# Performance work log

Hardware: AMD Instinct MI355X
Metric: run time of the kernel (lower is better)

## Reference

```python
import jax, jax.numpy as jnp
import numpy as np


def setup_inputs() -> dict:
    key = jax.random.key(0)
    k1, k2 = jax.random.split(key)
    L = 4096000  # 160^3 mesh points
    B = 64       # receivers
    # mesh coordinates in a 10m x 8m x 3m room
    mesh_3D = jax.random.uniform(k1, (L, 3), dtype=jnp.float32) * jnp.array([10.0, 8.0, 3.0], jnp.float32)
    receiver_pos = jax.random.uniform(k2, (B, 3), dtype=jnp.float32) * jnp.array([10.0, 8.0, 3.0], jnp.float32)
    return {"mesh_3D": mesh_3D, "receiver_pos": receiver_pos}


def reference(mesh_3D, receiver_pos):
    # mesh_3D: (L, 3) flattened meshgrid; receiver_pos: (B, 3)
    mesh_flat = mesh_3D.reshape(-1, 3)                      # (L, 3)
    L = mesh_flat.shape[0]
    # Brute-force squared distances via ||m||^2 - 2 m.r + ||r||^2 -> (B, L)
    # (sqrt is monotone, argmin unchanged; distances themselves are not returned)
    m_sq = jnp.sum(mesh_flat * mesh_flat, axis=1)           # (L,)
    r_sq = jnp.sum(receiver_pos * receiver_pos, axis=1)     # (B,)
    cross = receiver_pos @ mesh_flat.T                      # (B, L)
    d2 = m_sq[None, :] - 2.0 * cross + r_sq[:, None]        # (B, L)
    min_idx = jnp.argmin(d2, axis=1)                        # (B,)
    one_hot = jnp.zeros((L,), mesh_flat.dtype).at[min_idx].set(1.0)
    closest_points = mesh_flat[min_idx]                     # (B, 3)
    input_tensor = jnp.concatenate([mesh_flat, one_hot[:, None]], axis=1)  # (L, 4)
    return input_tensor, closest_points
```

## Files before the change

### kernel.cpp

```cpp
#include <hip/hip_runtime.h>
#include <cfloat>
#include <math.h>
#include <stdint.h>

#pragma clang fp contract(off)

#define RPW 16
#define NQ  256
#define PPL 8
#define TILESZ (256 * PPL)

__device__ __forceinline__ uint32_t monotone_key(float f) {
    uint32_t u = __float_as_uint(f);
    return (u & 0x80000000u) ? ~u : (u | 0x80000000u);
}

__device__ __forceinline__ float rfl_f(float x) {
    return __uint_as_float((uint32_t)__builtin_amdgcn_readfirstlane((int)__float_as_uint(x)));
}

__device__ __forceinline__ unsigned long long shfl_xor_u64(unsigned long long v, int m) {
    uint32_t lo = (uint32_t)v, hi = (uint32_t)(v >> 32);
    lo = (uint32_t)__shfl_xor((int)lo, m, 64);
    hi = (uint32_t)__shfl_xor((int)hi, m, 64);
    return ((unsigned long long)hi << 32) | lo;
}

__global__ void __launch_bounds__(256, 4) fused_kernel(
        const float* __restrict__ mesh, const float* __restrict__ recv,
        float* __restrict__ out, unsigned long long* __restrict__ ws,
        int L, int B, int ntiles) {
    __shared__ unsigned long long wmin[4][RPW];

    const int tid  = threadIdx.x;
    const int lane = tid & 63;
    const int wave = tid >> 6;
    const int rq   = blockIdx.x / NQ;
    const int q0   = blockIdx.x % NQ;

    float rx[RPW], ry[RPW], rz[RPW], rsq[RPW];
#pragma unroll
    for (int c = 0; c < RPW; ++c) {
        const int r = rq * RPW + c;
        float x = 0.f, y = 0.f, z = 0.f;
        if (r < B) {
            x = recv[r * 3 + 0];
            y = recv[r * 3 + 1];
            z = recv[r * 3 + 2];
        }
        rx[c]  = rfl_f(x);
        ry[c]  = rfl_f(y);
        rz[c]  = rfl_f(z);
        rsq[c] = rfl_f((x * x + y * y) + z * z);
    }

    float    best[RPW];
    uint32_t grp[RPW];
#pragma unroll
    for (int c = 0; c < RPW; ++c) { best[c] = FLT_MAX; grp[c] = 0; }

    const bool writer = (rq == 0);

    for (int t = q0; t < ntiles; t += NQ) {
        const int p0 = t * TILESZ + (wave << 9) + (lane << 3);
        float xs[PPL], ys[PPL], zs[PPL], ms[PPL];
        if (p0 + PPL <= L) {
            const float4* __restrict__ m4 = (const float4*)(mesh + (size_t)p0 * 3);
            const float4 fa = m4[0], fb = m4[1], fc = m4[2];
            const float4 fd = m4[3], fe = m4[4], ff = m4[5];
            if (writer) {
                float4* __restrict__ o4 = (float4*)(out + (size_t)p0 * 4);
                o4[0] = make_float4(fa.x, fa.y, fa.z, 0.f);
                o4[1] = make_float4(fa.w, fb.x, fb.y, 0.f);
                o4[2] = make_float4(fb.z, fb.w, fc.x, 0.f);
                o4[3] = make_float4(fc.y, fc.z, fc.w, 0.f);
                o4[4] = make_float4(fd.x, fd.y, fd.z, 0.f);
                o4[5] = make_float4(fd.w, fe.x, fe.y, 0.f);
                o4[6] = make_float4(fe.z, fe.w, ff.x, 0.f);
                o4[7] = make_float4(ff.y, ff.z, ff.w, 0.f);
            }
            xs[0] = fa.x; ys[0] = fa.y; zs[0] = fa.z;
            xs[1] = fa.w; ys[1] = fb.x; zs[1] = fb.y;
            xs[2] = fb.z; ys[2] = fb.w; zs[2] = fc.x;
            xs[3] = fc.y; ys[3] = fc.z; zs[3] = fc.w;
            xs[4] = fd.x; ys[4] = fd.y; zs[4] = fd.z;
            xs[5] = fd.w; ys[5] = fe.x; zs[5] = fe.y;
            xs[6] = fe.z; ys[6] = fe.w; zs[6] = ff.x;
            xs[7] = ff.y; ys[7] = ff.z; zs[7] = ff.w;
#pragma unroll
            for (int j = 0; j < PPL; ++j)
                ms[j] = (xs[j] * xs[j] + ys[j] * ys[j]) + zs[j] * zs[j];
        } else {
#pragma unroll
            for (int j = 0; j < PPL; ++j) {
                const int p = p0 + j;
                if (p < L) {
                    xs[j] = mesh[(size_t)p * 3 + 0];
                    ys[j] = mesh[(size_t)p * 3 + 1];
                    zs[j] = mesh[(size_t)p * 3 + 2];
                    ms[j] = (xs[j] * xs[j] + ys[j] * ys[j]) + zs[j] * zs[j];
                    if (writer) {
                        out[(size_t)p * 4 + 0] = xs[j];
                        out[(size_t)p * 4 + 1] = ys[j];
                        out[(size_t)p * 4 + 2] = zs[j];
                        out[(size_t)p * 4 + 3] = 0.f;
                    }
                } else {
                    xs[j] = 0.f; ys[j] = 0.f; zs[j] = 0.f;
                    ms[j] = INFINITY;
                }
            }
        }

        const uint32_t g = (uint32_t)(p0 >> 3);
#pragma unroll
        for (int c = 0; c < RPW; ++c) {
            float v[PPL];
#pragma unroll
            for (int j = 0; j < PPL; ++j) {
                float cr = fmaf(rz[c], zs[j], fmaf(ry[c], ys[j], rx[c] * xs[j]));
                v[j] = fmaf(-2.0f, cr, ms[j]);
            }
            float a  = fminf(fminf(v[0], v[1]), v[2]);
            float b  = fminf(fminf(v[3], v[4]), v[5]);
            float cc = fminf(v[6], v[7]);
            float tl = fminf(fminf(a, b), cc);
            float d2g = tl + rsq[c];
            if (d2g < best[c]) { best[c] = d2g; grp[c] = g; }
        }
    }

#pragma unroll
    for (int c = 0; c < RPW; ++c) {
        unsigned long long kk =
            ((unsigned long long)monotone_key(best[c]) << 32) | grp[c];
#pragma unroll
        for (int off = 32; off >= 1; off >>= 1) {
            unsigned long long o = shfl_xor_u64(kk, off);
            if (o < kk) kk = o;
        }
        if (lane == 0) wmin[wave][c] = kk;
    }
    __syncthreads();
    if (tid < RPW) {
        unsigned long long kk = wmin[0][tid];
#pragma unroll
        for (int w = 1; w < 4; ++w) {
            unsigned long long o = wmin[w][tid];
            if (o < kk) kk = o;
        }
        const int r = rq * RPW + tid;
        if (r < B) atomicMin(&ws[r], kk);
    }
}

__global__ void finalize_kernel(
        const float* __restrict__ mesh, const float* __restrict__ recv,
        const unsigned long long* __restrict__ ws,
        float* __restrict__ out, int L, int B) {
    const int r = threadIdx.x;
    if (r >= B) return;
    const unsigned long long key = ws[r];
    const int p0 = (int)(key & 0xFFFFFFFFull) << 3;

    const float rx = recv[r * 3 + 0];
    const float ry = recv[r * 3 + 1];
    const float rz = recv[r * 3 + 2];
    const float rsq = (rx * rx + ry * ry) + rz * rz;

    float bestd = FLT_MAX;
    int   bidx  = p0;
    for (int j = 0; j < 8; ++j) {
        const int p = p0 + j;
        float d2;
        if (p < L) {
            const float x = mesh[(size_t)p * 3 + 0];
            const float y = mesh[(size_t)p * 3 + 1];
            const float z = mesh[(size_t)p * 3 + 2];
            const float ms = (x * x + y * y) + z * z;
            const float cr = fmaf(rz, z, fmaf(ry, y, rx * x));
            d2 = fmaf(-2.0f, cr, ms) + rsq;
        } else {
            d2 = INFINITY;
        }
        if (d2 < bestd) { bestd = d2; bidx = p; }
    }

    out[(size_t)bidx * 4 + 3] = 1.0f;
    float* cp = out + (size_t)L * 4 + (size_t)r * 3;
    cp[0] = mesh[(size_t)bidx * 3 + 0];
    cp[1] = mesh[(size_t)bidx * 3 + 1];
    cp[2] = mesh[(size_t)bidx * 3 + 2];
}

extern "C" void kernel_launch(void* const* d_in, const int* in_sizes, int n_in,
                              void* d_out, int out_size, void* d_ws, size_t ws_size,
                              hipStream_t stream) {
    const float* mesh = (const float*)d_in[0];
    const float* recv = (const float*)d_in[1];
    float* out = (float*)d_out;
    const int L = in_sizes[0] / 3;
    const int B = in_sizes[1] / 3;
    unsigned long long* ws = (unsigned long long*)d_ws;

    hipMemsetAsync(ws, 0xFF, (size_t)B * sizeof(unsigned long long), stream);

    const int ntiles = (L + TILESZ - 1) / TILESZ;
    fused_kernel<<<4 * NQ, 256, 0, stream>>>(mesh, recv, out, ws, L, B, ntiles);

    finalize_kernel<<<1, 64, 0, stream>>>(mesh, recv, ws, out, L, B);
}
```

Measured before the change: 61.26 us.

## Use packed FP32 FMA math and prefetch next mesh tile into registers

Rewrites the per-receiver distance computation to use two-wide float vectors, so the compiler can emit packed FMA instructions that handle two mesh points per instruction. It also software-pipelines the tile loop by issuing the next tile's six float4 loads before the compute on the current tile, hiding global load latency. The cost is more live registers for the prefetched tile and packing shuffles, which could pressure occupancy under the 4-wave launch bound.

```diff
diff --git a/kernel.cpp b/kernel.cpp
--- a/kernel.cpp
+++ b/kernel.cpp
@@ -4,6 +4,8 @@
 #include <stdint.h>
 
 #pragma clang fp contract(off)
+
+typedef float v2f __attribute__((ext_vector_type(2)));
 
 #define RPW 16
 #define NQ  256
@@ -24,6 +26,11 @@
     lo = (uint32_t)__shfl_xor((int)lo, m, 64);
     hi = (uint32_t)__shfl_xor((int)hi, m, 64);
     return ((unsigned long long)hi << 32) | lo;
+}
+
+__device__ __forceinline__ v2f sp(float s) { return (v2f){s, s}; }
+__device__ __forceinline__ v2f pkfma(v2f a, v2f b, v2f c) {
+    return __builtin_elementwise_fma(a, b, c);
 }
 
 __global__ void __launch_bounds__(256, 4) fused_kernel(
@@ -61,73 +68,100 @@
 
     const bool writer = (rq == 0);
 
-    for (int t = q0; t < ntiles; t += NQ) {
-        const int p0 = t * TILESZ + (wave << 9) + (lane << 3);
-        float xs[PPL], ys[PPL], zs[PPL], ms[PPL];
-        if (p0 + PPL <= L) {
-            const float4* __restrict__ m4 = (const float4*)(mesh + (size_t)p0 * 3);
-            const float4 fa = m4[0], fb = m4[1], fc = m4[2];
-            const float4 fd = m4[3], fe = m4[4], ff = m4[5];
+    float4 nb0, nb1, nb2, nb3, nb4, nb5;
+    int  t  = q0;
+    int  p0 = t * TILESZ + (wave << 9) + (lane << 3);
+    bool curFull = (t < ntiles) && (p0 + PPL <= L);
+    if (curFull) {
+        const float4* __restrict__ m4 = (const float4*)(mesh + (size_t)p0 * 3);
+        nb0 = m4[0]; nb1 = m4[1]; nb2 = m4[2];
+        nb3 = m4[3]; nb4 = m4[4]; nb5 = m4[5];
+    }
+
+    while (t < ntiles) {
+        v2f x2[4], y2[4], z2[4], ms2[4];
+        if (curFull) {
+            x2[0] = (v2f){nb0.x, nb0.w}; y2[0] = (v2f){nb0.y, nb1.x}; z2[0] = (v2f){nb0.z, nb1.y};
+            x2[1] = (v2f){nb1.z, nb2.y}; y2[1] = (v2f){nb1.w, nb2.z}; z2[1] = (v2f){nb2.x, nb2.w};
+            x2[2] = (v2f){nb3.x, nb3.w}; y2[2] = (v2f){nb3.y, nb4.x}; z2[2] = (v2f){nb3.z, nb4.y};
+            x2[3] = (v2f){nb4.z, nb5.y}; y2[3] = (v2f){nb4.w, nb5.z}; z2[3] = (v2f){nb5.x, nb5.w};
+#pragma unroll
+            for (int j = 0; j < 4; ++j)
+                ms2[j] = (x2[j] * x2[j] + y2[j] * y2[j]) + z2[j] * z2[j];
             if (writer) {
                 float4* __restrict__ o4 = (float4*)(out + (size_t)p0 * 4);
-                o4[0] = make_float4(fa.x, fa.y, fa.z, 0.f);
-                o4[1] = make_float4(fa.w, fb.x, fb.y, 0.f);
-                o4[2] = make_float4(fb.z, fb.w, fc.x, 0.f);
-                o4[3] = make_float4(fc.y, fc.z, fc.w, 0.f);
-                o4[4] = make_float4(fd.x, fd.y, fd.z, 0.f);
-                o4[5] = make_float4(fd.w, fe.x, fe.y, 0.f);
-                o4[6] = make_float4(fe.z, fe.w, ff.x, 0.f);
-                o4[7] = make_float4(ff.y, ff.z, ff.w, 0.f);
+                o4[0] = make_float4(x2[0].x, y2[0].x, z2[0].x, 0.f);
+                o4[1] = make_float4(x2[0].y, y2[0].y, z2[0].y, 0.f);
+                o4[2] = make_float4(x2[1].x, y2[1].x, z2[1].x, 0.f);
+                o4[3] = make_float4(x2[1].y, y2[1].y, z2[1].y, 0.f);
+                o4[4] = make_float4(x2[2].x, y2[2].x, z2[2].x, 0.f);
+                o4[5] = make_float4(x2[2].y, y2[2].y, z2[2].y, 0.f);
+                o4[6] = make_float4(x2[3].x, y2[3].x, z2[3].x, 0.f);
+                o4[7] = make_float4(x2[3].y, y2[3].y, z2[3].y, 0.f);
             }
-            xs[0] = fa.x; ys[0] = fa.y; zs[0] = fa.z;
-            xs[1] = fa.w; ys[1] = fb.x; zs[1] = fb.y;
-            xs[2] = fb.z; ys[2] = fb.w; zs[2] = fc.x;
-            xs[3] = fc.y; ys[3] = fc.z; zs[3] = fc.w;
-            xs[4] = fd.x; ys[4] = fd.y; zs[4] = fd.z;
-            xs[5] = fd.w; ys[5] = fe.x; zs[5] = fe.y;
-            xs[6] = fe.z; ys[6] = fe.w; zs[6] = ff.x;
-            xs[7] = ff.y; ys[7] = ff.z; zs[7] = ff.w;
-#pragma unroll
-            for (int j = 0; j < PPL; ++j)
-                ms[j] = (xs[j] * xs[j] + ys[j] * ys[j]) + zs[j] * zs[j];
         } else {
+            float xx[PPL], yy[PPL], zz[PPL], mm[PPL];
 #pragma unroll
             for (int j = 0; j < PPL; ++j) {
                 const int p = p0 + j;
                 if (p < L) {
-                    xs[j] = mesh[(size_t)p * 3 + 0];
-                    ys[j] = mesh[(size_t)p * 3 + 1];
-                    zs[j] = mesh[(size_t)p * 3 + 2];
-                    ms[j] = (xs[j] * xs[j] + ys[j] * ys[j]) + zs[j] * zs[j];
+                    xx[j] = mesh[(size_t)p * 3 + 0];
+                    yy[j] = mesh[(size_t)p * 3 + 1];
+                    zz[j] = mesh[(size_t)p * 3 + 2];
+                    mm[j] = (xx[j] * xx[j] + yy[j] * yy[j]) + zz[j] * zz[j];
                     if (writer) {
-                        out[(size_t)p * 4 + 0] = xs[j];
-                        out[(size_t)p * 4 + 1] = ys[j];
-                        out[(size_t)p * 4 + 2] = zs[j];
+                        out[(size_t)p * 4 + 0] = xx[j];
+                        out[(size_t)p * 4 + 1] = yy[j];
+                        out[(size_t)p * 4 + 2] = zz[j];
                         out[(size_t)p * 4 + 3] = 0.f;
                     }
                 } else {
-                    xs[j] = 0.f; ys[j] = 0.f; zs[j] = 0.f;
-                    ms[j] = INFINITY;
+                    xx[j] = 0.f; yy[j] = 0.f; zz[j] = 0.f;
+                    mm[j] = INFINITY;
                 }
             }
+#pragma unroll
+            for (int j = 0; j < 4; ++j) {
+                x2[j]  = (v2f){xx[2 * j], xx[2 * j + 1]};
+                y2[j]  = (v2f){yy[2 * j], yy[2 * j + 1]};
+                z2[j]  = (v2f){zz[2 * j], zz[2 * j + 1]};
+                ms2[j] = (v2f){mm[2 * j], mm[2 * j + 1]};
+            }
+        }
+
+        const int  tn  = t + NQ;
+        const int  pn0 = tn * TILESZ + (wave << 9) + (lane << 3);
+        const bool nextFull = (tn < ntiles) && (pn0 + PPL <= L);
+        if (nextFull) {
+            const float4* __restrict__ m4 = (const float4*)(mesh + (size_t)pn0 * 3);
+            nb0 = m4[0]; nb1 = m4[1]; nb2 = m4[2];
+            nb3 = m4[3]; nb4 = m4[4]; nb5 = m4[5];
         }
 
         const uint32_t g = (uint32_t)(p0 >> 3);
 #pragma unroll
         for (int c = 0; c < RPW; ++c) {
-            float v[PPL];
-#pragma unroll
-            for (int j = 0; j < PPL; ++j) {
-                float cr = fmaf(rz[c], zs[j], fmaf(ry[c], ys[j], rx[c] * xs[j]));
-                v[j] = fmaf(-2.0f, cr, ms[j]);
-            }
-            float a  = fminf(fminf(v[0], v[1]), v[2]);
-            float b  = fminf(fminf(v[3], v[4]), v[5]);
-            float cc = fminf(v[6], v[7]);
+            v2f vA = pkfma(sp(-2.0f),
+                           pkfma(sp(rz[c]), z2[0], pkfma(sp(ry[c]), y2[0], sp(rx[c]) * x2[0])),
+                           ms2[0]);
+            v2f vB = pkfma(sp(-2.0f),
+                           pkfma(sp(rz[c]), z2[1], pkfma(sp(ry[c]), y2[1], sp(rx[c]) * x2[1])),
+                           ms2[1]);
+            v2f vC = pkfma(sp(-2.0f),
+                           pkfma(sp(rz[c]), z2[2], pkfma(sp(ry[c]), y2[2], sp(rx[c]) * x2[2])),
+                           ms2[2]);
+            v2f vD = pkfma(sp(-2.0f),
+                           pkfma(sp(rz[c]), z2[3], pkfma(sp(ry[c]), y2[3], sp(rx[c]) * x2[3])),
+                           ms2[3]);
+            float a  = fminf(fminf(vA.x, vA.y), vB.x);
+            float b  = fminf(fminf(vB.y, vC.x), vC.y);
+            float cc = fminf(vD.x, vD.y);
             float tl = fminf(fminf(a, b), cc);
             float d2g = tl + rsq[c];
             if (d2g < best[c]) { best[c] = d2g; grp[c] = g; }
         }
+
+        t = tn; p0 = pn0; curFull = nextFull;
     }
 
 #pragma unroll
```

New measurement: 58.05 us. -5.2%, faster.
